# Kernel tuning notes

Measured on AMD Instinct MI355X. Metric: run time of the kernel, lower is better.

The kernel has to match this reference:

```python
import jax, jax.numpy as jnp
import numpy as np

N_NODES = 100000
N_EDGES = 1600000
IN_DIM = 128
HIDDEN = 128
EPS = 1e-5  # BatchNorm1d default eps


def gcn_conv(x, src, dst, W, b, n_nodes):
    """PyG GCNConv with default add_self_loops=True, edge_weight=None.
    out = D^{-1/2} (A + I) D^{-1/2} X W + b, deg computed from dst (col)."""
    xw = x @ W  # [N, out_dim] -- transform before propagate, as in PyG
    ones = jnp.ones((src.shape[0],), dtype=x.dtype)
    deg = jax.ops.segment_sum(ones, dst, num_segments=n_nodes) + 1.0  # +1 self-loop
    dis = jax.lax.rsqrt(deg)  # deg >= 1 always
    norm = dis[src] * dis[dst]  # [E]
    msgs = xw[src] * norm[:, None]  # [E, out_dim] gather (irregular access)
    agg = jax.ops.segment_sum(msgs, dst, num_segments=n_nodes)
    agg = agg + xw * (1.0 / deg)[:, None]  # self-loop contribution, norm = 1/deg_i
    return agg + b


def batch_norm(x, gamma, beta):
    # training-mode BatchNorm1d: biased batch statistics over the node dim
    m = jnp.mean(x, axis=0)
    v = jnp.mean(jnp.square(x - m), axis=0)
    return gamma * (x - m) * jax.lax.rsqrt(v + EPS) + beta


def setup_inputs() -> dict:
    key = jax.random.key(0)
    ks = jax.random.split(key, 6)
    x = jax.random.normal(ks[0], (N_NODES, IN_DIM), dtype=jnp.float32)
    edge_index = jax.random.randint(ks[1], (2, N_EDGES), 0, N_NODES, dtype=jnp.int64)
    # Glorot-ish scaled weights
    W1 = jax.random.normal(ks[2], (IN_DIM, HIDDEN), dtype=jnp.float32) / np.sqrt(IN_DIM)
    W2 = jax.random.normal(ks[3], (HIDDEN, HIDDEN // 2), dtype=jnp.float32) / np.sqrt(HIDDEN)
    Wf = jax.random.normal(ks[4], (HIDDEN // 2, 1), dtype=jnp.float32) / np.sqrt(HIDDEN // 2)
    return {
        "x": x,
        "edge_index": edge_index,
        "W1": W1, "b1": jnp.zeros((HIDDEN,), jnp.float32),
        "g1": jnp.ones((HIDDEN,), jnp.float32), "beta1": jnp.zeros((HIDDEN,), jnp.float32),
        "W2": W2, "b2": jnp.zeros((HIDDEN // 2,), jnp.float32),
        "g2": jnp.ones((HIDDEN // 2,), jnp.float32), "beta2": jnp.zeros((HIDDEN // 2,), jnp.float32),
        "Wf": Wf, "bf": jnp.zeros((1,), jnp.float32),
    }


def reference(x, edge_index, W1, b1, g1, beta1, W2, b2, g2, beta2, Wf, bf):
    src, dst = edge_index[0], edge_index[1]
    n = x.shape[0]
    h = jax.nn.relu(batch_norm(gcn_conv(x, src, dst, W1, b1, n), g1, beta1))
    # dropout is identity in eval / correctness-baseline mode
    h = jax.nn.relu(batch_norm(gcn_conv(h, src, dst, W2, b2, n), g2, beta2))
    return h @ Wf + bf  # [N, 1]
```

## Files before the change

### kernel.cpp

```cpp
#include <hip/hip_runtime.h>

#define NN 100000
#define NE 1600000
#define D1 128
#define D2 64
#define BN_EPS 1e-5f
#define SCAN_CHUNK 512
#define NB_SCAN ((NN + SCAN_CHUNK - 1) / SCAN_CHUNK)

typedef unsigned int uint32;
typedef unsigned long long u64;
typedef unsigned short ushort;
typedef __attribute__((ext_vector_type(8))) short bf16x8;
typedef __attribute__((ext_vector_type(4))) float f32x4;

__device__ __forceinline__ ushort f2bf1(float f) {
    uint32 u = __float_as_uint(f);
    return (ushort)((u + 0x7FFFu + ((u >> 16) & 1u)) >> 16);
}
__device__ __forceinline__ uint32 f2bf_pair(float a, float b) {
    uint32 ua = __float_as_uint(a), ub = __float_as_uint(b);
    ua = (ua + 0x7FFFu + ((ua >> 16) & 1u)) >> 16;
    ub = (ub + 0x7FFFu + ((ub >> 16) & 1u)) >> 16;
    return ua | (ub << 16);
}
__device__ __forceinline__ float bf_lo(uint32 v) { return __uint_as_float(v << 16); }
__device__ __forceinline__ float bf_hi(uint32 v) { return __uint_as_float(v & 0xFFFF0000u); }

__global__ __launch_bounds__(256) void cnt_k(const int* __restrict__ dst,
                                             int* __restrict__ cnt) {
    int i = blockIdx.x * 256 + threadIdx.x;
    if (i < NE) atomicAdd(&cnt[dst[i]], 1);
}

__global__ __launch_bounds__(256) void make_dis_k(const int* __restrict__ cnt,
                                                  float* __restrict__ dis) {
    int i = blockIdx.x * 256 + threadIdx.x;
    if (i < NN) dis[i] = rsqrtf((float)cnt[i] + 1.0f);
}

__global__ __launch_bounds__(SCAN_CHUNK) void scan1_k(const int* __restrict__ cnt,
                                                      int* __restrict__ rowptr,
                                                      int* __restrict__ bsum) {
    __shared__ int sh[SCAN_CHUNK];
    int tid = threadIdx.x;
    int g = blockIdx.x * SCAN_CHUNK + tid;
    int v = (g < NN) ? cnt[g] : 0;
    sh[tid] = v;
    __syncthreads();
    for (int o = 1; o < SCAN_CHUNK; o <<= 1) {
        int t = (tid >= o) ? sh[tid - o] : 0;
        __syncthreads();
        sh[tid] += t;
        __syncthreads();
    }
    if (g < NN) rowptr[g] = sh[tid] - v;
    if (tid == SCAN_CHUNK - 1) bsum[blockIdx.x] = sh[tid];
}

__global__ void scan2_k(int* __restrict__ bsum) {
    if (threadIdx.x == 0 && blockIdx.x == 0) {
        int a = 0;
        for (int i = 0; i < NB_SCAN; ++i) { int t = bsum[i]; bsum[i] = a; a += t; }
    }
}

__global__ __launch_bounds__(256) void scan3_k(int* __restrict__ rowptr,
                                               const int* __restrict__ bsum) {
    int g = blockIdx.x * 256 + threadIdx.x;
    if (g < NN) rowptr[g] += bsum[g >> 9];
    if (g == 0) rowptr[NN] = NE;
}

__global__ __launch_bounds__(256) void fill_k(const int* __restrict__ src,
                                              const int* __restrict__ dst,
                                              const int* __restrict__ rowptr,
                                              const float* __restrict__ dis,
                                              int* __restrict__ cur,
                                              int* __restrict__ esrc,
                                              float* __restrict__ ew) {
    int e = blockIdx.x * 256 + threadIdx.x;
    if (e >= NE) return;
    int d = dst[e];
    int s = src[e];
    int p = rowptr[d] + atomicAdd(&cur[d], 1);
    esrc[p] = s;
    ew[p] = dis[s] * dis[d];
}

__global__ void bncoef_k(const float* __restrict__ sums, const float* __restrict__ ssq,
                         const float* __restrict__ g, const float* __restrict__ beta,
                         float* __restrict__ coef, int dim) {
    int c = threadIdx.x;
    if (c >= dim) return;
    float m = sums[c] * (1.0f / NN);
    float var = ssq[c] * (1.0f / NN) - m * m;
    float sc = g[c] * rsqrtf(var + BN_EPS);
    coef[c] = sc;
    coef[dim + c] = beta[c] - m * sc;
}

__global__ __launch_bounds__(256) void wt_k(const float* __restrict__ W1,
                                            const float* __restrict__ W2,
                                            ushort* __restrict__ wt1,
                                            ushort* __restrict__ wt2) {
    int i = blockIdx.x * 256 + threadIdx.x;
    if (i < 128 * 128) {
        int c = i >> 7, k = i & 127;
        wt1[i] = f2bf1(W1[k * 128 + c]);
    } else if (i < 128 * 128 + 64 * 128) {
        int o = i - 128 * 128;
        int c = o >> 7, k = o & 127;
        wt2[o] = f2bf1(W2[k * 64 + c]);
    }
}

template<int OUT, bool BF16BN>
__global__ __launch_bounds__(256) void mgemm_k(const void* __restrict__ Xv,
                                               const ushort* __restrict__ Wt,
                                               const float* __restrict__ coef,
                                               ushort* __restrict__ Yb) {
    const int lane = threadIdx.x & 63;
    const int wv = threadIdx.x >> 6;
    const int row0 = blockIdx.x * 64 + wv * 16;
    const int m = lane & 15;
    const int kg = lane >> 4;
    const int rowA = min(row0 + m, NN - 1);
    f32x4 acc[OUT / 16];
    #pragma unroll
    for (int t = 0; t < OUT / 16; ++t) acc[t] = (f32x4){0.f, 0.f, 0.f, 0.f};

    #pragma unroll
    for (int kc = 0; kc < 128; kc += 32) {
        const int k0 = kc + kg * 8;
        float xs[8];
        if constexpr (BF16BN) {
            const ushort* Xb = (const ushort*)Xv;
            uint4 raw = *(const uint4*)(Xb + (size_t)rowA * 128 + k0);
            xs[0] = bf_lo(raw.x); xs[1] = bf_hi(raw.x);
            xs[2] = bf_lo(raw.y); xs[3] = bf_hi(raw.y);
            xs[4] = bf_lo(raw.z); xs[5] = bf_hi(raw.z);
            xs[6] = bf_lo(raw.w); xs[7] = bf_hi(raw.w);
            float4 sa = *(const float4*)(coef + k0);
            float4 sb = *(const float4*)(coef + k0 + 4);
            float4 ha = *(const float4*)(coef + 128 + k0);
            float4 hb = *(const float4*)(coef + 128 + k0 + 4);
            xs[0] = fmaxf(fmaf(xs[0], sa.x, ha.x), 0.f);
            xs[1] = fmaxf(fmaf(xs[1], sa.y, ha.y), 0.f);
            xs[2] = fmaxf(fmaf(xs[2], sa.z, ha.z), 0.f);
            xs[3] = fmaxf(fmaf(xs[3], sa.w, ha.w), 0.f);
            xs[4] = fmaxf(fmaf(xs[4], sb.x, hb.x), 0.f);
            xs[5] = fmaxf(fmaf(xs[5], sb.y, hb.y), 0.f);
            xs[6] = fmaxf(fmaf(xs[6], sb.z, hb.z), 0.f);
            xs[7] = fmaxf(fmaf(xs[7], sb.w, hb.w), 0.f);
        } else {
            const float* X = (const float*)Xv;
            float4 xa = *(const float4*)(X + (size_t)rowA * 128 + k0);
            float4 xb = *(const float4*)(X + (size_t)rowA * 128 + k0 + 4);
            xs[0] = xa.x; xs[1] = xa.y; xs[2] = xa.z; xs[3] = xa.w;
            xs[4] = xb.x; xs[5] = xb.y; xs[6] = xb.z; xs[7] = xb.w;
        }
        bf16x8 af;
        #pragma unroll
        for (int i = 0; i < 8; ++i) af[i] = (short)f2bf1(xs[i]);
        #pragma unroll
        for (int t = 0; t < OUT / 16; ++t) {
            bf16x8 bfr = *(const bf16x8*)(Wt + (size_t)(t * 16 + m) * 128 + k0);
            acc[t] = __builtin_amdgcn_mfma_f32_16x16x32_bf16(af, bfr, acc[t], 0, 0, 0);
        }
    }
    #pragma unroll
    for (int t = 0; t < OUT / 16; ++t) {
        #pragma unroll
        for (int r = 0; r < 4; ++r) {
            int rr = row0 + kg * 4 + r;
            if (rr < NN) Yb[(size_t)rr * OUT + t * 16 + m] = f2bf1(acc[t][r]);
        }
    }
}

__global__ __launch_bounds__(256) void agg128_k(const int* __restrict__ rowptr,
                                                const int* __restrict__ esrc,
                                                const float* __restrict__ ew,
                                                const float* __restrict__ dis,
                                                const uint32* __restrict__ xwb,
                                                const float* __restrict__ b,
                                                uint32* __restrict__ agg1b,
                                                float* __restrict__ sums,
                                                float* __restrict__ ssq) {
    const int lane = threadIdx.x & 63;
    const int wid = (blockIdx.x * 256 + threadIdx.x) >> 6;
    const int nwaves = gridDim.x * 4;
    float s0 = 0.f, s1 = 0.f, q0 = 0.f, q1 = 0.f;
    const float bc0 = b[lane * 2], bc1 = b[lane * 2 + 1];

    for (int n = wid; n < NN; n += nwaves) {
        const int beg = rowptr[n], end = rowptr[n + 1];
        const float dn = dis[n];
        float ax = 0.f, ay = 0.f;
        int e = beg;
        for (; e + 8 <= end; e += 8) {
            int idx[8]; float w[8]; uint32 vv[8];
            #pragma unroll
            for (int j = 0; j < 8; ++j) idx[j] = esrc[e + j];
            #pragma unroll
            for (int j = 0; j < 8; ++j) w[j] = ew[e + j];
            #pragma unroll
            for (int j = 0; j < 8; ++j)
                vv[j] = xwb[(size_t)idx[j] * 64 + lane];
            #pragma unroll
            for (int j = 0; j < 8; ++j) {
                ax = fmaf(bf_lo(vv[j]), w[j], ax);
                ay = fmaf(bf_hi(vv[j]), w[j], ay);
            }
        }
        for (; e < end; ++e) {
            int s = esrc[e];
            float w = ew[e];
            uint32 v = xwb[(size_t)s * 64 + lane];
            ax = fmaf(bf_lo(v), w, ax);
            ay = fmaf(bf_hi(v), w, ay);
        }
        float sl = dn * dn;
        uint32 xv = xwb[(size_t)n * 64 + lane];
        ax = fmaf(bf_lo(xv), sl, ax) + bc0;
        ay = fmaf(bf_hi(xv), sl, ay) + bc1;
        agg1b[(size_t)n * 64 + lane] = f2bf_pair(ax, ay);
        s0 += ax; q0 = fmaf(ax, ax, q0);
        s1 += ay; q1 = fmaf(ay, ay, q1);
    }

    __shared__ float ls[256];
    ls[threadIdx.x] = 0.f;
    __syncthreads();
    atomicAdd(&ls[lane * 2], s0);
    atomicAdd(&ls[lane * 2 + 1], s1);
    atomicAdd(&ls[128 + lane * 2], q0);
    atomicAdd(&ls[128 + lane * 2 + 1], q1);
    __syncthreads();
    if (threadIdx.x < 128) atomicAdd(&sums[threadIdx.x], ls[threadIdx.x]);
    else atomicAdd(&ssq[threadIdx.x - 128], ls[threadIdx.x]);
}

__global__ __launch_bounds__(256) void agg64_k(const int* __restrict__ rowptr,
                                               const int* __restrict__ esrc,
                                               const float* __restrict__ ew,
                                               const float* __restrict__ dis,
                                               const uint32* __restrict__ xwb,
                                               const float* __restrict__ b,
                                               float* __restrict__ agg,
                                               float* __restrict__ sums,
                                               float* __restrict__ ssq) {
    const int lane = threadIdx.x & 63;
    const int half = lane >> 5;
    const int sl = lane & 31;
    const int wid = (blockIdx.x * 256 + threadIdx.x) >> 6;
    const int nwaves = gridDim.x * 4;
    float s0 = 0.f, s1 = 0.f, q0 = 0.f, q1 = 0.f;
    const float bc0 = b[sl * 2], bc1 = b[sl * 2 + 1];

    for (int n = wid; n < NN; n += nwaves) {
        const int beg = rowptr[n], end = rowptr[n + 1];
        const float dn = dis[n];
        float ax = 0.f, ay = 0.f;
        int e = beg;
        for (; e + 16 <= end; e += 16) {
            int idx[8]; float w[8]; uint32 vv[8];
            #pragma unroll
            for (int j = 0; j < 8; ++j) idx[j] = esrc[e + 2 * j + half];
            #pragma unroll
            for (int j = 0; j < 8; ++j) w[j] = ew[e + 2 * j + half];
            #pragma unroll
            for (int j = 0; j < 8; ++j)
                vv[j] = xwb[(size_t)idx[j] * 32 + sl];
            #pragma unroll
            for (int j = 0; j < 8; ++j) {
                ax = fmaf(bf_lo(vv[j]), w[j], ax);
                ay = fmaf(bf_hi(vv[j]), w[j], ay);
            }
        }
        for (; e + 2 <= end; e += 2) {
            int s = esrc[e + half];
            float w = ew[e + half];
            uint32 v = xwb[(size_t)s * 32 + sl];
            ax = fmaf(bf_lo(v), w, ax);
            ay = fmaf(bf_hi(v), w, ay);
        }
        if (e < end && half == 0) {
            int s = esrc[e];
            float w = ew[e];
            uint32 v = xwb[(size_t)s * 32 + sl];
            ax = fmaf(bf_lo(v), w, ax);
            ay = fmaf(bf_hi(v), w, ay);
        }
        ax += __shfl_down(ax, 32);
        ay += __shfl_down(ay, 32);
        if (half == 0) {
            float slf = dn * dn;
            uint32 xv = xwb[(size_t)n * 32 + sl];
            ax = fmaf(bf_lo(xv), slf, ax) + bc0;
            ay = fmaf(bf_hi(xv), slf, ay) + bc1;
            *(float2*)&agg[(size_t)n * 64 + sl * 2] = make_float2(ax, ay);
            s0 += ax; q0 = fmaf(ax, ax, q0);
            s1 += ay; q1 = fmaf(ay, ay, q1);
        }
    }

    __shared__ float ls[128];
    if (threadIdx.x < 128) ls[threadIdx.x] = 0.f;
    __syncthreads();
    if (half == 0) {
        atomicAdd(&ls[sl * 2], s0);
        atomicAdd(&ls[sl * 2 + 1], s1);
        atomicAdd(&ls[64 + sl * 2], q0);
        atomicAdd(&ls[64 + sl * 2 + 1], q1);
    }
    __syncthreads();
    if (threadIdx.x < 64) atomicAdd(&sums[threadIdx.x], ls[threadIdx.x]);
    else if (threadIdx.x < 128) atomicAdd(&ssq[threadIdx.x - 64], ls[threadIdx.x]);
}

__global__ __launch_bounds__(256) void final_k(const float* __restrict__ h,
                                               const float* __restrict__ coef,
                                               const float* __restrict__ Wf,
                                               const float* __restrict__ bf,
                                               float* __restrict__ out) {
    int wid = (blockIdx.x * 256 + threadIdx.x) >> 6;
    int lane = threadIdx.x & 63;
    if (wid >= NN) return;
    float v = fmaxf(fmaf(h[(size_t)wid * 64 + lane], coef[lane], coef[64 + lane]), 0.f)
              * Wf[lane];
    #pragma unroll
    for (int o = 32; o > 0; o >>= 1) v += __shfl_down(v, o);
    if (lane == 0) out[wid] = v + bf[0];
}

extern "C" void kernel_launch(void* const* d_in, const int* in_sizes, int n_in,
                              void* d_out, int out_size, void* d_ws, size_t ws_size,
                              hipStream_t stream) {
    const float* x   = (const float*)d_in[0];
    const int*   ei  = (const int*)d_in[1];
    const int*   src = ei;
    const int*   dst = ei + NE;
    const float* W1  = (const float*)d_in[2];
    const float* b1  = (const float*)d_in[3];
    const float* g1  = (const float*)d_in[4];
    const float* be1 = (const float*)d_in[5];
    const float* W2  = (const float*)d_in[6];
    const float* b2  = (const float*)d_in[7];
    const float* g2  = (const float*)d_in[8];
    const float* be2 = (const float*)d_in[9];
    const float* Wf  = (const float*)d_in[10];
    const float* bf  = (const float*)d_in[11];
    float* out = (float*)d_out;

    uint32* xwb   = (uint32*)d_ws;
    uint32* agg1b = xwb + (size_t)NN * 64;
    float*  agg2  = (float*)(agg1b + (size_t)NN * 64);
    float*  dis   = agg2 + (size_t)NN * D2;
    float*  sums1 = dis + NN;
    float*  ssq1  = sums1 + D1;
    float*  sums2 = ssq1 + D1;
    float*  ssq2  = sums2 + D2;
    float*  coef1 = ssq2 + D2;
    float*  coef2 = coef1 + 2 * D1;
    ushort* wt1   = (ushort*)(coef2 + 2 * D2);
    ushort* wt2   = wt1 + 128 * 128;
    int*    cnt    = (int*)(wt2 + 64 * 128);
    int*    cur    = cnt + NN;
    int*    rowptr = cur + NN;
    int*    bsum   = rowptr + NN + 1;
    int*    esrc   = bsum + 256;
    float*  ew     = (float*)(esrc + NE);

    hipMemsetAsync(cnt, 0, sizeof(int) * 2 * NN, stream);
    hipMemsetAsync(sums1, 0, sizeof(float) * (2 * D1 + 2 * D2), stream);

    cnt_k<<<(NE + 255) / 256, 256, 0, stream>>>(dst, cnt);
    make_dis_k<<<(NN + 255) / 256, 256, 0, stream>>>(cnt, dis);
    scan1_k<<<NB_SCAN, SCAN_CHUNK, 0, stream>>>(cnt, rowptr, bsum);
    scan2_k<<<1, 64, 0, stream>>>(bsum);
    scan3_k<<<(NN + 255) / 256, 256, 0, stream>>>(rowptr, bsum);
    fill_k<<<(NE + 255) / 256, 256, 0, stream>>>(src, dst, rowptr, dis, cur, esrc, ew);
    wt_k<<<(128 * 128 + 64 * 128 + 255) / 256, 256, 0, stream>>>(W1, W2, wt1, wt2);

    mgemm_k<128, false><<<(NN + 63) / 64, 256, 0, stream>>>(x, wt1, nullptr, (ushort*)xwb);
    agg128_k<<<2048, 256, 0, stream>>>(rowptr, esrc, ew, dis, xwb, b1, agg1b, sums1, ssq1);
    bncoef_k<<<1, 128, 0, stream>>>(sums1, ssq1, g1, be1, coef1, D1);

    mgemm_k<64, true><<<(NN + 63) / 64, 256, 0, stream>>>(agg1b, wt2, coef1, (ushort*)xwb);
    agg64_k<<<2048, 256, 0, stream>>>(rowptr, esrc, ew, dis, xwb, b2, agg2, sums2, ssq2);
    bncoef_k<<<1, 64, 0, stream>>>(sums2, ssq2, g2, be2, coef2, D2);

    final_k<<<(NN * 64 + 255) / 256, 256, 0, stream>>>(agg2, coef2, Wf, bf, out);
}
```

Measured before the change: 446.7 us.

## Slice aggregation by feature columns across blocks and compute edge weights on the fly

Replaces the two per-node-per-wave aggregation kernels with one templated kernel. Each block now handles a 16-column feature slice, and each wave processes 8 edges in parallel, with 8 lanes per edge reading 32-byte segments. Partial sums are then reduced with shuffles. The precomputed per-edge weight array is removed: weights are recomputed as dis[src]*dis[dst] at gather time, which saves the ew write in fill_k and the ew reads in aggregation but adds an extra random dis gather per edge. The column slicing is meant to shrink the working set each block touches so gathers hit in cache, at the cost of reading the row pointers and edge indices once per slice.

```diff
diff --git a/kernel.cpp b/kernel.cpp
--- a/kernel.cpp
+++ b/kernel.cpp
@@ -9,7 +9,6 @@
 #define NB_SCAN ((NN + SCAN_CHUNK - 1) / SCAN_CHUNK)
 
 typedef unsigned int uint32;
-typedef unsigned long long u64;
 typedef unsigned short ushort;
 typedef __attribute__((ext_vector_type(8))) short bf16x8;
 typedef __attribute__((ext_vector_type(4))) float f32x4;
@@ -75,17 +74,14 @@
 __global__ __launch_bounds__(256) void fill_k(const int* __restrict__ src,
                                               const int* __restrict__ dst,
                                               const int* __restrict__ rowptr,
-                                              const float* __restrict__ dis,
                                               int* __restrict__ cur,
-                                              int* __restrict__ esrc,
-                                              float* __restrict__ ew) {
+                                              int* __restrict__ esrc) {
     int e = blockIdx.x * 256 + threadIdx.x;
     if (e >= NE) return;
     int d = dst[e];
     int s = src[e];
     int p = rowptr[d] + atomicAdd(&cur[d], 1);
     esrc[p] = s;
-    ew[p] = dis[s] * dis[d];
 }
 
 __global__ void bncoef_k(const float* __restrict__ sums, const float* __restrict__ ssq,
@@ -179,145 +175,82 @@
     }
 }
 
-__global__ __launch_bounds__(256) void agg128_k(const int* __restrict__ rowptr,
-                                                const int* __restrict__ esrc,
-                                                const float* __restrict__ ew,
-                                                const float* __restrict__ dis,
-                                                const uint32* __restrict__ xwb,
-                                                const float* __restrict__ b,
-                                                uint32* __restrict__ agg1b,
-                                                float* __restrict__ sums,
-                                                float* __restrict__ ssq) {
+template<int DIM>
+__global__ __launch_bounds__(256) void aggs_k(const int* __restrict__ rowptr,
+                                              const int* __restrict__ esrc,
+                                              const float* __restrict__ dis,
+                                              const uint32* __restrict__ xwb,
+                                              const float* __restrict__ b,
+                                              void* __restrict__ aggout,
+                                              float* __restrict__ sums,
+                                              float* __restrict__ ssq) {
+    constexpr int SLICES = DIM / 16;
+    constexpr int LOG2S = (DIM == 128) ? 3 : 2;
+    constexpr int RU = DIM / 2;
+    const int slice = blockIdx.x & (SLICES - 1);
     const int lane = threadIdx.x & 63;
-    const int wid = (blockIdx.x * 256 + threadIdx.x) >> 6;
-    const int nwaves = gridDim.x * 4;
+    const int g = lane >> 3;
+    const int c8 = lane & 7;
+    const int cp = slice * 8 + c8;
+    const int wv = threadIdx.x >> 6;
+    const int n0 = ((int)blockIdx.x >> LOG2S) * 4 + wv;
+    const int nstride = ((int)gridDim.x >> LOG2S) * 4;
     float s0 = 0.f, s1 = 0.f, q0 = 0.f, q1 = 0.f;
-    const float bc0 = b[lane * 2], bc1 = b[lane * 2 + 1];
-
-    for (int n = wid; n < NN; n += nwaves) {
-        const int beg = rowptr[n], end = rowptr[n + 1];
-        const float dn = dis[n];
-        float ax = 0.f, ay = 0.f;
-        int e = beg;
-        for (; e + 8 <= end; e += 8) {
-            int idx[8]; float w[8]; uint32 vv[8];
-            #pragma unroll
-            for (int j = 0; j < 8; ++j) idx[j] = esrc[e + j];
-            #pragma unroll
-            for (int j = 0; j < 8; ++j) w[j] = ew[e + j];
-            #pragma unroll
-            for (int j = 0; j < 8; ++j)
-                vv[j] = xwb[(size_t)idx[j] * 64 + lane];
-            #pragma unroll
-            for (int j = 0; j < 8; ++j) {
-                ax = fmaf(bf_lo(vv[j]), w[j], ax);
-                ay = fmaf(bf_hi(vv[j]), w[j], ay);
-            }
-        }
-        for (; e < end; ++e) {
-            int s = esrc[e];
-            float w = ew[e];
-            uint32 v = xwb[(size_t)s * 64 + lane];
-            ax = fmaf(bf_lo(v), w, ax);
-            ay = fmaf(bf_hi(v), w, ay);
-        }
-        float sl = dn * dn;
-        uint32 xv = xwb[(size_t)n * 64 + lane];
-        ax = fmaf(bf_lo(xv), sl, ax) + bc0;
-        ay = fmaf(bf_hi(xv), sl, ay) + bc1;
-        agg1b[(size_t)n * 64 + lane] = f2bf_pair(ax, ay);
-        s0 += ax; q0 = fmaf(ax, ax, q0);
-        s1 += ay; q1 = fmaf(ay, ay, q1);
-    }
-
-    __shared__ float ls[256];
-    ls[threadIdx.x] = 0.f;
-    __syncthreads();
-    atomicAdd(&ls[lane * 2], s0);
-    atomicAdd(&ls[lane * 2 + 1], s1);
-    atomicAdd(&ls[128 + lane * 2], q0);
-    atomicAdd(&ls[128 + lane * 2 + 1], q1);
-    __syncthreads();
-    if (threadIdx.x < 128) atomicAdd(&sums[threadIdx.x], ls[threadIdx.x]);
-    else atomicAdd(&ssq[threadIdx.x - 128], ls[threadIdx.x]);
-}
-
-__global__ __launch_bounds__(256) void agg64_k(const int* __restrict__ rowptr,
-                                               const int* __restrict__ esrc,
-                                               const float* __restrict__ ew,
-                                               const float* __restrict__ dis,
-                                               const uint32* __restrict__ xwb,
-                                               const float* __restrict__ b,
-                                               float* __restrict__ agg,
-                                               float* __restrict__ sums,
-                                               float* __restrict__ ssq) {
-    const int lane = threadIdx.x & 63;
-    const int half = lane >> 5;
-    const int sl = lane & 31;
-    const int wid = (blockIdx.x * 256 + threadIdx.x) >> 6;
-    const int nwaves = gridDim.x * 4;
-    float s0 = 0.f, s1 = 0.f, q0 = 0.f, q1 = 0.f;
-    const float bc0 = b[sl * 2], bc1 = b[sl * 2 + 1];
-
-    for (int n = wid; n < NN; n += nwaves) {
+    const float bc0 = b[cp * 2], bc1 = b[cp * 2 + 1];
+
+    for (int n = n0; n < NN; n += nstride) {
         const int beg = rowptr[n], end = rowptr[n + 1];
         const float dn = dis[n];
         float ax = 0.f, ay = 0.f;
         int e = beg;
         for (; e + 16 <= end; e += 16) {
-            int idx[8]; float w[8]; uint32 vv[8];
-            #pragma unroll
-            for (int j = 0; j < 8; ++j) idx[j] = esrc[e + 2 * j + half];
-            #pragma unroll
-            for (int j = 0; j < 8; ++j) w[j] = ew[e + 2 * j + half];
-            #pragma unroll
-            for (int j = 0; j < 8; ++j)
-                vv[j] = xwb[(size_t)idx[j] * 32 + sl];
-            #pragma unroll
-            for (int j = 0; j < 8; ++j) {
-                ax = fmaf(bf_lo(vv[j]), w[j], ax);
-                ay = fmaf(bf_hi(vv[j]), w[j], ay);
-            }
-        }
-        for (; e + 2 <= end; e += 2) {
-            int s = esrc[e + half];
-            float w = ew[e + half];
-            uint32 v = xwb[(size_t)s * 32 + sl];
+            int sa = __builtin_nontemporal_load(&esrc[e + g]);
+            int sb = __builtin_nontemporal_load(&esrc[e + 8 + g]);
+            float wa = dis[sa] * dn;
+            float wb = dis[sb] * dn;
+            uint32 va = xwb[(size_t)sa * RU + cp];
+            uint32 vb = xwb[(size_t)sb * RU + cp];
+            ax = fmaf(bf_lo(va), wa, ax); ay = fmaf(bf_hi(va), wa, ay);
+            ax = fmaf(bf_lo(vb), wb, ax); ay = fmaf(bf_hi(vb), wb, ay);
+        }
+        for (; e < end; e += 8) {
+            int ee = e + g;
+            bool msk = ee < end;
+            int s = msk ? __builtin_nontemporal_load(&esrc[ee]) : 0;
+            float w = msk ? dis[s] * dn : 0.f;
+            uint32 v = xwb[(size_t)s * RU + cp];
             ax = fmaf(bf_lo(v), w, ax);
             ay = fmaf(bf_hi(v), w, ay);
         }
-        if (e < end && half == 0) {
-            int s = esrc[e];
-            float w = ew[e];
-            uint32 v = xwb[(size_t)s * 32 + sl];
-            ax = fmaf(bf_lo(v), w, ax);
-            ay = fmaf(bf_hi(v), w, ay);
-        }
-        ax += __shfl_down(ax, 32);
-        ay += __shfl_down(ay, 32);
-        if (half == 0) {
-            float slf = dn * dn;
-            uint32 xv = xwb[(size_t)n * 32 + sl];
-            ax = fmaf(bf_lo(xv), slf, ax) + bc0;
-            ay = fmaf(bf_hi(xv), slf, ay) + bc1;
-            *(float2*)&agg[(size_t)n * 64 + sl * 2] = make_float2(ax, ay);
+        ax += __shfl_down(ax, 32); ay += __shfl_down(ay, 32);
+        ax += __shfl_down(ax, 16); ay += __shfl_down(ay, 16);
+        ax += __shfl_down(ax, 8);  ay += __shfl_down(ay, 8);
+        if (lane < 8) {
+            float sl = dn * dn;
+            uint32 xv = xwb[(size_t)n * RU + cp];
+            ax = fmaf(bf_lo(xv), sl, ax) + bc0;
+            ay = fmaf(bf_hi(xv), sl, ay) + bc1;
+            if constexpr (DIM == 128)
+                ((uint32*)aggout)[(size_t)n * RU + cp] = f2bf_pair(ax, ay);
+            else
+                ((float2*)aggout)[(size_t)n * 32 + cp] = make_float2(ax, ay);
             s0 += ax; q0 = fmaf(ax, ax, q0);
             s1 += ay; q1 = fmaf(ay, ay, q1);
         }
     }
 
-    __shared__ float ls[128];
-    if (threadIdx.x < 128) ls[threadIdx.x] = 0.f;
+    __shared__ float ls[32];
+    if (threadIdx.x < 32) ls[threadIdx.x] = 0.f;
     __syncthreads();
-    if (half == 0) {
-        atomicAdd(&ls[sl * 2], s0);
-        atomicAdd(&ls[sl * 2 + 1], s1);
-        atomicAdd(&ls[64 + sl * 2], q0);
-        atomicAdd(&ls[64 + sl * 2 + 1], q1);
+    if (lane < 8) {
+        atomicAdd(&ls[c8 * 2], s0);
+        atomicAdd(&ls[c8 * 2 + 1], s1);
+        atomicAdd(&ls[16 + c8 * 2], q0);
+        atomicAdd(&ls[16 + c8 * 2 + 1], q1);
     }
     __syncthreads();
-    if (threadIdx.x < 64) atomicAdd(&sums[threadIdx.x], ls[threadIdx.x]);
-    else if (threadIdx.x < 128) atomicAdd(&ssq[threadIdx.x - 64], ls[threadIdx.x]);
+    if (threadIdx.x < 16) atomicAdd(&sums[slice * 16 + threadIdx.x], ls[threadIdx.x]);
+    else if (threadIdx.x < 32) atomicAdd(&ssq[slice * 16 + threadIdx.x - 16], ls[threadIdx.x]);
 }
 
 __global__ __launch_bounds__(256) void final_k(const float* __restrict__ h,
@@ -371,7 +304,6 @@
     int*    rowptr = cur + NN;
     int*    bsum   = rowptr + NN + 1;
     int*    esrc   = bsum + 256;
-    float*  ew     = (float*)(esrc + NE);
 
     hipMemsetAsync(cnt, 0, sizeof(int) * 2 * NN, stream);
     hipMemsetAsync(sums1, 0, sizeof(float) * (2 * D1 + 2 * D2), stream);
@@ -381,15 +313,15 @@
     scan1_k<<<NB_SCAN, SCAN_CHUNK, 0, stream>>>(cnt, rowptr, bsum);
     scan2_k<<<1, 64, 0, stream>>>(bsum);
     scan3_k<<<(NN + 255) / 256, 256, 0, stream>>>(rowptr, bsum);
-    fill_k<<<(NE + 255) / 256, 256, 0, stream>>>(src, dst, rowptr, dis, cur, esrc, ew);
+    fill_k<<<(NE + 255) / 256, 256, 0, stream>>>(src, dst, rowptr, cur, esrc);
     wt_k<<<(128 * 128 + 64 * 128 + 255) / 256, 256, 0, stream>>>(W1, W2, wt1, wt2);
 
     mgemm_k<128, false><<<(NN + 63) / 64, 256, 0, stream>>>(x, wt1, nullptr, (ushort*)xwb);
-    agg128_k<<<2048, 256, 0, stream>>>(rowptr, esrc, ew, dis, xwb, b1, agg1b, sums1, ssq1);
+    aggs_k<128><<<2048, 256, 0, stream>>>(rowptr, esrc, dis, xwb, b1, agg1b, sums1, ssq1);
     bncoef_k<<<1, 128, 0, stream>>>(sums1, ssq1, g1, be1, coef1, D1);
 
     mgemm_k<64, true><<<(NN + 63) / 64, 256, 0, stream>>>(agg1b, wt2, coef1, (ushort*)xwb);
-    agg64_k<<<2048, 256, 0, stream>>>(rowptr, esrc, ew, dis, xwb, b2, agg2, sums2, ssq2);
+    aggs_k<64><<<2048, 256, 0, stream>>>(rowptr, esrc, dis, xwb, b2, agg2, sums2, ssq2);
     bncoef_k<<<1, 64, 0, stream>>>(sums2, ssq2, g2, be2, coef2, D2);
 
     final_k<<<(NN * 64 + 255) / 256, 256, 0, stream>>>(agg2, coef2, Wf, bf, out);
```

After: 813.5 us. 82.1% more time.

## Fold tiny kernels into neighbors and store layer-2 aggregate as bf16

Applied to the files above, without the earlier changes.

Computes the degree normalisation inside the scan kernel, and computes BatchNorm coefficients in each block of the following GEMM and final kernels, which removes three small launches. The two memsets become one. The layer-2 aggregate is written as packed bf16 instead of fp32, and the final kernel handles two nodes per wavefront, which reduces memory traffic. The cost is redundant per-block coefficient work and extra rounding of the second-layer activations.

```diff
diff --git a/kernel.cpp b/kernel.cpp
--- a/kernel.cpp
+++ b/kernel.cpp
@@ -9,7 +9,6 @@
 #define NB_SCAN ((NN + SCAN_CHUNK - 1) / SCAN_CHUNK)
 
 typedef unsigned int uint32;
-typedef unsigned long long u64;
 typedef unsigned short ushort;
 typedef __attribute__((ext_vector_type(8))) short bf16x8;
 typedef __attribute__((ext_vector_type(4))) float f32x4;
@@ -33,19 +32,15 @@
     if (i < NE) atomicAdd(&cnt[dst[i]], 1);
 }
 
-__global__ __launch_bounds__(256) void make_dis_k(const int* __restrict__ cnt,
-                                                  float* __restrict__ dis) {
-    int i = blockIdx.x * 256 + threadIdx.x;
-    if (i < NN) dis[i] = rsqrtf((float)cnt[i] + 1.0f);
-}
-
 __global__ __launch_bounds__(SCAN_CHUNK) void scan1_k(const int* __restrict__ cnt,
                                                       int* __restrict__ rowptr,
-                                                      int* __restrict__ bsum) {
+                                                      int* __restrict__ bsum,
+                                                      float* __restrict__ dis) {
     __shared__ int sh[SCAN_CHUNK];
     int tid = threadIdx.x;
     int g = blockIdx.x * SCAN_CHUNK + tid;
     int v = (g < NN) ? cnt[g] : 0;
+    if (g < NN) dis[g] = rsqrtf((float)v + 1.0f);
     sh[tid] = v;
     __syncthreads();
     for (int o = 1; o < SCAN_CHUNK; o <<= 1) {
@@ -88,18 +83,6 @@
     ew[p] = dis[s] * dis[d];
 }
 
-__global__ void bncoef_k(const float* __restrict__ sums, const float* __restrict__ ssq,
-                         const float* __restrict__ g, const float* __restrict__ beta,
-                         float* __restrict__ coef, int dim) {
-    int c = threadIdx.x;
-    if (c >= dim) return;
-    float m = sums[c] * (1.0f / NN);
-    float var = ssq[c] * (1.0f / NN) - m * m;
-    float sc = g[c] * rsqrtf(var + BN_EPS);
-    coef[c] = sc;
-    coef[dim + c] = beta[c] - m * sc;
-}
-
 __global__ __launch_bounds__(256) void wt_k(const float* __restrict__ W1,
                                             const float* __restrict__ W2,
                                             ushort* __restrict__ wt1,
@@ -115,68 +98,110 @@
     }
 }
 
-template<int OUT, bool BF16BN>
-__global__ __launch_bounds__(256) void mgemm_k(const void* __restrict__ Xv,
-                                               const ushort* __restrict__ Wt,
-                                               const float* __restrict__ coef,
-                                               ushort* __restrict__ Yb) {
+__global__ __launch_bounds__(256) void mgemm1_k(const float* __restrict__ X,
+                                                const ushort* __restrict__ Wt,
+                                                ushort* __restrict__ Yb) {
     const int lane = threadIdx.x & 63;
     const int wv = threadIdx.x >> 6;
     const int row0 = blockIdx.x * 64 + wv * 16;
     const int m = lane & 15;
     const int kg = lane >> 4;
     const int rowA = min(row0 + m, NN - 1);
-    f32x4 acc[OUT / 16];
-    #pragma unroll
-    for (int t = 0; t < OUT / 16; ++t) acc[t] = (f32x4){0.f, 0.f, 0.f, 0.f};
+    f32x4 acc[8];
+    #pragma unroll
+    for (int t = 0; t < 8; ++t) acc[t] = (f32x4){0.f, 0.f, 0.f, 0.f};
 
     #pragma unroll
     for (int kc = 0; kc < 128; kc += 32) {
         const int k0 = kc + kg * 8;
+        float4 xa = *(const float4*)(X + (size_t)rowA * 128 + k0);
+        float4 xb = *(const float4*)(X + (size_t)rowA * 128 + k0 + 4);
+        bf16x8 af;
+        af[0] = (short)f2bf1(xa.x); af[1] = (short)f2bf1(xa.y);
+        af[2] = (short)f2bf1(xa.z); af[3] = (short)f2bf1(xa.w);
+        af[4] = (short)f2bf1(xb.x); af[5] = (short)f2bf1(xb.y);
+        af[6] = (short)f2bf1(xb.z); af[7] = (short)f2bf1(xb.w);
+        #pragma unroll
+        for (int t = 0; t < 8; ++t) {
+            bf16x8 bfr = *(const bf16x8*)(Wt + (size_t)(t * 16 + m) * 128 + k0);
+            acc[t] = __builtin_amdgcn_mfma_f32_16x16x32_bf16(af, bfr, acc[t], 0, 0, 0);
+        }
+    }
+    #pragma unroll
+    for (int t = 0; t < 8; ++t)
+        #pragma unroll
+        for (int r = 0; r < 4; ++r) {
+            int rr = row0 + kg * 4 + r;
+            if (rr < NN) Yb[(size_t)rr * 128 + t * 16 + m] = f2bf1(acc[t][r]);
+        }
+}
+
+__global__ __launch_bounds__(256) void mgemm2_k(const ushort* __restrict__ Xb,
+                                                const ushort* __restrict__ Wt,
+                                                const float* __restrict__ sums,
+                                                const float* __restrict__ ssq,
+                                                const float* __restrict__ g,
+                                                const float* __restrict__ beta,
+                                                ushort* __restrict__ Yb) {
+    __shared__ float sc[128], shf[128];
+    {
+        int t = threadIdx.x;
+        if (t < 128) {
+            float m = sums[t] * (1.0f / NN);
+            float var = ssq[t] * (1.0f / NN) - m * m;
+            float s = g[t] * rsqrtf(var + BN_EPS);
+            sc[t] = s;
+            shf[t] = beta[t] - m * s;
+        }
+    }
+    __syncthreads();
+    const int lane = threadIdx.x & 63;
+    const int wv = threadIdx.x >> 6;
+    const int row0 = blockIdx.x * 64 + wv * 16;
+    const int m = lane & 15;
+    const int kg = lane >> 4;
+    const int rowA = min(row0 + m, NN - 1);
+    f32x4 acc[4];
+    #pragma unroll
+    for (int t = 0; t < 4; ++t) acc[t] = (f32x4){0.f, 0.f, 0.f, 0.f};
+
+    #pragma unroll
+    for (int kc = 0; kc < 128; kc += 32) {
+        const int k0 = kc + kg * 8;
+        uint4 raw = *(const uint4*)(Xb + (size_t)rowA * 128 + k0);
         float xs[8];
-        if constexpr (BF16BN) {
-            const ushort* Xb = (const ushort*)Xv;
-            uint4 raw = *(const uint4*)(Xb + (size_t)rowA * 128 + k0);
-            xs[0] = bf_lo(raw.x); xs[1] = bf_hi(raw.x);
-            xs[2] = bf_lo(raw.y); xs[3] = bf_hi(raw.y);
-            xs[4] = bf_lo(raw.z); xs[5] = bf_hi(raw.z);
-            xs[6] = bf_lo(raw.w); xs[7] = bf_hi(raw.w);
-            float4 sa = *(const float4*)(coef + k0);
-            float4 sb = *(const float4*)(coef + k0 + 4);
-            float4 ha = *(const float4*)(coef + 128 + k0);
-            float4 hb = *(const float4*)(coef + 128 + k0 + 4);
-            xs[0] = fmaxf(fmaf(xs[0], sa.x, ha.x), 0.f);
-            xs[1] = fmaxf(fmaf(xs[1], sa.y, ha.y), 0.f);
-            xs[2] = fmaxf(fmaf(xs[2], sa.z, ha.z), 0.f);
-            xs[3] = fmaxf(fmaf(xs[3], sa.w, ha.w), 0.f);
-            xs[4] = fmaxf(fmaf(xs[4], sb.x, hb.x), 0.f);
-            xs[5] = fmaxf(fmaf(xs[5], sb.y, hb.y), 0.f);
-            xs[6] = fmaxf(fmaf(xs[6], sb.z, hb.z), 0.f);
-            xs[7] = fmaxf(fmaf(xs[7], sb.w, hb.w), 0.f);
-        } else {
-            const float* X = (const float*)Xv;
-            float4 xa = *(const float4*)(X + (size_t)rowA * 128 + k0);
-            float4 xb = *(const float4*)(X + (size_t)rowA * 128 + k0 + 4);
-            xs[0] = xa.x; xs[1] = xa.y; xs[2] = xa.z; xs[3] = xa.w;
-            xs[4] = xb.x; xs[5] = xb.y; xs[6] = xb.z; xs[7] = xb.w;
-        }
+        xs[0] = bf_lo(raw.x); xs[1] = bf_hi(raw.x);
+        xs[2] = bf_lo(raw.y); xs[3] = bf_hi(raw.y);
+        xs[4] = bf_lo(raw.z); xs[5] = bf_hi(raw.z);
+        xs[6] = bf_lo(raw.w); xs[7] = bf_hi(raw.w);
+        float4 sa = *(const float4*)&sc[k0];
+        float4 sb = *(const float4*)&sc[k0 + 4];
+        float4 ha = *(const float4*)&shf[k0];
+        float4 hb = *(const float4*)&shf[k0 + 4];
+        xs[0] = fmaxf(fmaf(xs[0], sa.x, ha.x), 0.f);
+        xs[1] = fmaxf(fmaf(xs[1], sa.y, ha.y), 0.f);
+        xs[2] = fmaxf(fmaf(xs[2], sa.z, ha.z), 0.f);
+        xs[3] = fmaxf(fmaf(xs[3], sa.w, ha.w), 0.f);
+        xs[4] = fmaxf(fmaf(xs[4], sb.x, hb.x), 0.f);
+        xs[5] = fmaxf(fmaf(xs[5], sb.y, hb.y), 0.f);
+        xs[6] = fmaxf(fmaf(xs[6], sb.z, hb.z), 0.f);
+        xs[7] = fmaxf(fmaf(xs[7], sb.w, hb.w), 0.f);
         bf16x8 af;
         #pragma unroll
         for (int i = 0; i < 8; ++i) af[i] = (short)f2bf1(xs[i]);
         #pragma unroll
-        for (int t = 0; t < OUT / 16; ++t) {
+        for (int t = 0; t < 4; ++t) {
             bf16x8 bfr = *(const bf16x8*)(Wt + (size_t)(t * 16 + m) * 128 + k0);
             acc[t] = __builtin_amdgcn_mfma_f32_16x16x32_bf16(af, bfr, acc[t], 0, 0, 0);
         }
     }
     #pragma unroll
-    for (int t = 0; t < OUT / 16; ++t) {
+    for (int t = 0; t < 4; ++t)
         #pragma unroll
         for (int r = 0; r < 4; ++r) {
             int rr = row0 + kg * 4 + r;
-            if (rr < NN) Yb[(size_t)rr * OUT + t * 16 + m] = f2bf1(acc[t][r]);
-        }
-    }
+            if (rr < NN) Yb[(size_t)rr * 64 + t * 16 + m] = f2bf1(acc[t][r]);
+        }
 }
 
 __global__ __launch_bounds__(256) void agg128_k(const int* __restrict__ rowptr,
@@ -248,7 +273,7 @@
                                                const float* __restrict__ dis,
                                                const uint32* __restrict__ xwb,
                                                const float* __restrict__ b,
-                                               float* __restrict__ agg,
+                                               uint32* __restrict__ agg2b,
                                                float* __restrict__ sums,
                                                float* __restrict__ ssq) {
     const int lane = threadIdx.x & 63;
@@ -300,7 +325,7 @@
             uint32 xv = xwb[(size_t)n * 32 + sl];
             ax = fmaf(bf_lo(xv), slf, ax) + bc0;
             ay = fmaf(bf_hi(xv), slf, ay) + bc1;
-            *(float2*)&agg[(size_t)n * 64 + sl * 2] = make_float2(ax, ay);
+            agg2b[(size_t)n * 32 + sl] = f2bf_pair(ax, ay);
             s0 += ax; q0 = fmaf(ax, ax, q0);
             s1 += ay; q1 = fmaf(ay, ay, q1);
         }
@@ -320,19 +345,38 @@
     else if (threadIdx.x < 128) atomicAdd(&ssq[threadIdx.x - 64], ls[threadIdx.x]);
 }
 
-__global__ __launch_bounds__(256) void final_k(const float* __restrict__ h,
-                                               const float* __restrict__ coef,
+__global__ __launch_bounds__(256) void final_k(const uint32* __restrict__ h2b,
+                                               const float* __restrict__ sums,
+                                               const float* __restrict__ ssq,
+                                               const float* __restrict__ g,
+                                               const float* __restrict__ beta,
                                                const float* __restrict__ Wf,
                                                const float* __restrict__ bf,
                                                float* __restrict__ out) {
-    int wid = (blockIdx.x * 256 + threadIdx.x) >> 6;
-    int lane = threadIdx.x & 63;
-    if (wid >= NN) return;
-    float v = fmaxf(fmaf(h[(size_t)wid * 64 + lane], coef[lane], coef[64 + lane]), 0.f)
-              * Wf[lane];
-    #pragma unroll
-    for (int o = 32; o > 0; o >>= 1) v += __shfl_down(v, o);
-    if (lane == 0) out[wid] = v + bf[0];
+    __shared__ float sc[64], shf[64];
+    {
+        int t = threadIdx.x;
+        if (t < 64) {
+            float m = sums[t] * (1.0f / NN);
+            float var = ssq[t] * (1.0f / NN) - m * m;
+            float s = g[t] * rsqrtf(var + BN_EPS);
+            sc[t] = s;
+            shf[t] = beta[t] - m * s;
+        }
+    }
+    __syncthreads();
+    const int lane = threadIdx.x & 63;
+    const int half = lane >> 5;
+    const int sl = lane & 31;
+    const int node = ((blockIdx.x * 256 + threadIdx.x) >> 6) * 2 + half;
+    if (node >= NN) return;
+    uint32 p = h2b[(size_t)node * 32 + sl];
+    float2 wf = *(const float2*)&Wf[sl * 2];
+    float v = fmaxf(fmaf(bf_lo(p), sc[sl * 2], shf[sl * 2]), 0.f) * wf.x;
+    v = fmaf(fmaxf(fmaf(bf_hi(p), sc[sl * 2 + 1], shf[sl * 2 + 1]), 0.f), wf.y, v);
+    #pragma unroll
+    for (int o = 16; o > 0; o >>= 1) v += __shfl_down(v, o, 32);
+    if (sl == 0) out[node] = v + bf[0];
 }
 
 extern "C" void kernel_launch(void* const* d_in, const int* in_sizes, int n_in,
@@ -356,41 +400,36 @@
 
     uint32* xwb   = (uint32*)d_ws;
     uint32* agg1b = xwb + (size_t)NN * 64;
-    float*  agg2  = (float*)(agg1b + (size_t)NN * 64);
-    float*  dis   = agg2 + (size_t)NN * D2;
-    float*  sums1 = dis + NN;
-    float*  ssq1  = sums1 + D1;
-    float*  sums2 = ssq1 + D1;
-    float*  ssq2  = sums2 + D2;
-    float*  coef1 = ssq2 + D2;
-    float*  coef2 = coef1 + 2 * D1;
-    ushort* wt1   = (ushort*)(coef2 + 2 * D2);
+    uint32* agg2b = agg1b + (size_t)NN * 64;
+    float*  dis   = (float*)(agg2b + (size_t)NN * 32);
+    ushort* wt1   = (ushort*)(dis + NN);
     ushort* wt2   = wt1 + 128 * 128;
-    int*    cnt    = (int*)(wt2 + 64 * 128);
-    int*    cur    = cnt + NN;
-    int*    rowptr = cur + NN;
+    int*    rowptr = (int*)(wt2 + 64 * 128);
     int*    bsum   = rowptr + NN + 1;
     int*    esrc   = bsum + 256;
     float*  ew     = (float*)(esrc + NE);
-
-    hipMemsetAsync(cnt, 0, sizeof(int) * 2 * NN, stream);
-    hipMemsetAsync(sums1, 0, sizeof(float) * (2 * D1 + 2 * D2), stream);
+    int*    cnt    = (int*)(ew + NE);
+    int*    cur    = cnt + NN;
+    float*  sums1  = (float*)(cur + NN);
+    float*  ssq1   = sums1 + D1;
+    float*  sums2  = ssq1 + D1;
+    float*  ssq2   = sums2 + D2;
+
+    hipMemsetAsync(cnt, 0, sizeof(int) * (2 * NN + 2 * D1 + 2 * D2), stream);
 
     cnt_k<<<(NE + 255) / 256, 256, 0, stream>>>(dst, cnt);
-    make_dis_k<<<(NN + 255) / 256, 256, 0, stream>>>(cnt, dis);
-    scan1_k<<<NB_SCAN, SCAN_CHUNK, 0, stream>>>(cnt, rowptr, bsum);
+    scan1_k<<<NB_SCAN, SCAN_CHUNK, 0, stream>>>(cnt, rowptr, bsum, dis);
     scan2_k<<<1, 64, 0, stream>>>(bsum);
     scan3_k<<<(NN + 255) / 256, 256, 0, stream>>>(rowptr, bsum);
     fill_k<<<(NE + 255) / 256, 256, 0, stream>>>(src, dst, rowptr, dis, cur, esrc, ew);
     wt_k<<<(128 * 128 + 64 * 128 + 255) / 256, 256, 0, stream>>>(W1, W2, wt1, wt2);
 
-    mgemm_k<128, false><<<(NN + 63) / 64, 256, 0, stream>>>(x, wt1, nullptr, (ushort*)xwb);
+    mgemm1_k<<<(NN + 63) / 64, 256, 0, stream>>>(x, wt1, (ushort*)xwb);
     agg128_k<<<2048, 256, 0, stream>>>(rowptr, esrc, ew, dis, xwb, b1, agg1b, sums1, ssq1);
-    bncoef_k<<<1, 128, 0, stream>>>(sums1, ssq1, g1, be1, coef1, D1);
-
-    mgemm_k<64, true><<<(NN + 63) / 64, 256, 0, stream>>>(agg1b, wt2, coef1, (ushort*)xwb);
-    agg64_k<<<2048, 256, 0, stream>>>(rowptr, esrc, ew, dis, xwb, b2, agg2, sums2, ssq2);
-    bncoef_k<<<1, 64, 0, stream>>>(sums2, ssq2, g2, be2, coef2, D2);
-
-    final_k<<<(NN * 64 + 255) / 256, 256, 0, stream>>>(agg2, coef2, Wf, bf, out);
-}
+
+    mgemm2_k<<<(NN + 63) / 64, 256, 0, stream>>>((const ushort*)agg1b, wt2, sums1, ssq1,
+                                                 g1, be1, (ushort*)xwb);
+    agg64_k<<<2048, 256, 0, stream>>>(rowptr, esrc, ew, dis, xwb, b2, agg2b, sums2, ssq2);
+
+    final_k<<<(NN / 2 + 3) / 4, 256, 0, stream>>>(agg2b, sums2, ssq2, g2, be2, Wf, bf, out);
+}
```

Result: slower. 472.7 us (+5.8%).
